# Performance work log

Hardware: AMD Instinct MI355X
Metric: run time of the kernel (lower is better)

The kernel has to match this reference:

```python
import jax, jax.numpy as jnp
import numpy as np

N_NODES = 50000
N_EDGES = 800000
F_IN, HID, N_CLS = 128, 64, 40


def gcn_conv(x, edge_index, W, b):
    """PyG GCNConv: add self-loops, symmetric normalization, linear, aggregate, bias."""
    n = x.shape[0]
    loop = jnp.arange(n, dtype=edge_index.dtype)
    src = jnp.concatenate([edge_index[0], loop])  # [E+N]
    dst = jnp.concatenate([edge_index[1], loop])  # [E+N]
    deg = jax.ops.segment_sum(jnp.ones_like(dst, dtype=x.dtype), dst, num_segments=n)
    dinv = jnp.where(deg > 0, jax.lax.rsqrt(deg), 0.0)
    norm = dinv[src] * dinv[dst]                   # [E+N]
    h = x @ W                                      # [N, out]
    out = jax.ops.segment_sum(h[src] * norm[:, None], dst, num_segments=n)
    return out + b


def setup_inputs() -> dict:
    key = jax.random.key(0)
    k1, k2, k3, k4 = jax.random.split(key, 4)
    x = jax.random.normal(k1, (N_NODES, F_IN), dtype=jnp.float32)
    edge_index = jax.random.randint(k2, (2, N_EDGES), 0, N_NODES, dtype=jnp.int32)
    W1 = jax.random.normal(k3, (F_IN, HID), dtype=jnp.float32) / np.sqrt(F_IN)
    b1 = jnp.zeros((HID,), dtype=jnp.float32)
    W2 = jax.random.normal(k4, (HID, N_CLS), dtype=jnp.float32) / np.sqrt(HID)
    b2 = jnp.zeros((N_CLS,), dtype=jnp.float32)
    return {"x": x, "edge_index": edge_index, "W1": W1, "b1": b1, "W2": W2, "b2": b2}


def reference(x, edge_index, W1, b1, W2, b2):
    # layer 1: GCNConv -> ReLU -> Dropout(eval = identity)
    h = jax.nn.relu(gcn_conv(x, edge_index, W1, b1))
    # layer 2: GCNConv -> ReLU -> Dropout(eval = identity); return_logits=True
    h = jax.nn.relu(gcn_conv(h, edge_index, W2, b2))
    return h
```

## Files before the change

### kernel.cpp

```cpp
#include <hip/hip_runtime.h>
#include <hip/hip_bf16.h>
#include <hip/hip_fp16.h>


#define N_FEAT_IN 128
#define N_HID 64
#define N_CLS 40

__device__ __forceinline__ float4 h4_to_f4(uint2 u) {
    __half2 a = *(__half2*)&u.x;
    __half2 b = *(__half2*)&u.y;
    float2 fa = __half22float2(a);
    float2 fb = __half22float2(b);
    return make_float4(fa.x, fa.y, fb.x, fb.y);
}

__device__ __forceinline__ uint2 f4_to_h4(float4 v) {
    uint2 w;
    *(__half2*)&w.x = __floats2half2_rn(v.x, v.y);
    *(__half2*)&w.y = __floats2half2_rn(v.z, v.w);
    return w;
}

__global__ void k_zero(int* a, int n) {
    int i = blockIdx.x * blockDim.x + threadIdx.x;
    if (i < n) a[i] = 0;
}

__global__ void k_count(const int* __restrict__ ei, int* deg, int* __restrict__ rank,
                        int E) {
    int e = blockIdx.x * blockDim.x + threadIdx.x;
    if (e < E) rank[e] = atomicAdd(&deg[ei[E + e]], 1);
}

__global__ void k_scan1(const int* __restrict__ deg, float* __restrict__ dinv,
                        int* incl, int* blksum, int n) {
    __shared__ int s[256];
    int i = blockIdx.x * 256 + threadIdx.x;
    int v = (i < n) ? deg[i] : 0;
    if (i < n) dinv[i] = 1.0f / sqrtf((float)(v + 1));
    s[threadIdx.x] = v;
    __syncthreads();
    for (int off = 1; off < 256; off <<= 1) {
        int t = (threadIdx.x >= off) ? s[threadIdx.x - off] : 0;
        __syncthreads();
        s[threadIdx.x] += t;
        __syncthreads();
    }
    if (i < n) incl[i] = s[threadIdx.x];
    if (threadIdx.x == 255) blksum[blockIdx.x] = s[255];
}

__global__ void k_scanB(const int* __restrict__ blksum, const int* __restrict__ incl,
                        const int* __restrict__ deg, int* __restrict__ row_start,
                        int nb, int n) {
    __shared__ int s[256];
    int t = threadIdx.x;
    int v = (t < nb) ? blksum[t] : 0;
    s[t] = v;
    __syncthreads();
    for (int off = 1; off < 256; off <<= 1) {
        int u = (t >= off) ? s[t - off] : 0;
        __syncthreads();
        s[t] += u;
        __syncthreads();
    }
    int bid = blockIdx.x;
    int blkoff = (bid == 0) ? 0 : s[bid - 1];
    int i = bid * 256 + t;
    if (i < n) row_start[i] = incl[i] - deg[i] + blkoff;
    if (bid == 0 && t == 0) row_start[n] = s[nb - 1];
}

__global__ __launch_bounds__(256) void k_g1_scatter2(
    const float* __restrict__ x, const float* __restrict__ W,
    const float* __restrict__ dinv, __half* __restrict__ hs, int n, int gb,
    const int* __restrict__ ei, const int* __restrict__ rank,
    const int* __restrict__ row_start, int* __restrict__ csr_src, int E) {
    __shared__ float Wl[64 * 64];
    __shared__ float Xs[64 * 68];
    int t = threadIdx.x;
    if (blockIdx.x >= gb) {
        int e = (blockIdx.x - gb) * 256 + t;
        if (e < E) {
            int s = ei[e];
            int d = ei[E + e];
            csr_src[row_start[d] + rank[e]] = s;
        }
        return;
    }
    int node0 = blockIdx.x * 64;
    int tn = t & 15;
    int tc = t >> 4;
    float acc[4][4] = {};
    for (int p = 0; p < 2; ++p) {
#pragma unroll
        for (int i = 0; i < 4; ++i) {
            int r = (t >> 4) + 16 * i;
            int c4 = t & 15;
            *(float4*)&Wl[r * 64 + c4 * 4] =
                *(const float4*)&W[(p * 64 + r) * N_HID + c4 * 4];
            int gr = node0 + r;
            float4 v = (gr < n)
                ? *(const float4*)&x[(size_t)gr * N_FEAT_IN + p * 64 + c4 * 4]
                : make_float4(0.f, 0.f, 0.f, 0.f);
            *(float4*)&Xs[r * 68 + c4 * 4] = v;
        }
        __syncthreads();
        for (int k = 0; k < 64; k += 4) {
            float4 xa[4], wb[4];
#pragma unroll
            for (int i = 0; i < 4; ++i)
                xa[i] = *(float4*)&Xs[(tn + 16 * i) * 68 + k];
#pragma unroll
            for (int kk = 0; kk < 4; ++kk)
                wb[kk] = *(float4*)&Wl[(k + kk) * 64 + tc * 4];
#pragma unroll
            for (int kk = 0; kk < 4; ++kk)
#pragma unroll
                for (int i = 0; i < 4; ++i)
#pragma unroll
                    for (int j = 0; j < 4; ++j)
                        acc[i][j] += ((const float*)&xa[i])[kk] * ((const float*)&wb[kk])[j];
        }
        __syncthreads();
    }
#pragma unroll
    for (int i = 0; i < 4; ++i) {
        int gr = node0 + tn + 16 * i;
        if (gr < n) {
            float di = dinv[gr];
            float4 v = make_float4(acc[i][0] * di, acc[i][1] * di,
                                   acc[i][2] * di, acc[i][3] * di);
            *(uint2*)(hs + (size_t)gr * N_HID + tc * 4) = f4_to_h4(v);
        }
    }
}

template <bool L1>
__global__ __launch_bounds__(256) void k_aggrh(const int* __restrict__ row_start,
                                               const int* __restrict__ csr_src,
                                               const float* __restrict__ dinv,
                                               const __half* __restrict__ hs,
                                               const float* __restrict__ b,
                                               void* __restrict__ outp, int n) {
    __shared__ int Ss[4 * 64];
    int wv = threadIdx.x >> 6, lane = threadIdx.x & 63;
    int g = lane >> 4, l = lane & 15;
    int node = blockIdx.x * 4 + wv;
    if (node >= n) return;
    float4 acc = make_float4(0.f, 0.f, 0.f, 0.f);
    if (g == 0) {
        uint2 u = *(const uint2*)(hs + (size_t)node * N_HID + l * 4);
        acc = h4_to_f4(u);
    }
    int beg = row_start[node], end = row_start[node + 1];
    for (int j0 = beg; j0 < end; j0 += 64) {
        int j = j0 + lane;
        if (j < end) Ss[wv * 64 + lane] = csr_src[j];
        int cnt = min(64, end - j0);
        int t = 0;
        for (; t + 16 <= cnt; t += 16) {
            int s1 = Ss[wv * 64 + t + g];
            int s2 = Ss[wv * 64 + t + 4 + g];
            int s3 = Ss[wv * 64 + t + 8 + g];
            int s4 = Ss[wv * 64 + t + 12 + g];
            uint2 u1 = *(const uint2*)(hs + (size_t)s1 * N_HID + l * 4);
            uint2 u2 = *(const uint2*)(hs + (size_t)s2 * N_HID + l * 4);
            uint2 u3 = *(const uint2*)(hs + (size_t)s3 * N_HID + l * 4);
            uint2 u4 = *(const uint2*)(hs + (size_t)s4 * N_HID + l * 4);
            float4 v1 = h4_to_f4(u1), v2 = h4_to_f4(u2);
            float4 v3 = h4_to_f4(u3), v4 = h4_to_f4(u4);
            acc.x += (v1.x + v2.x) + (v3.x + v4.x);
            acc.y += (v1.y + v2.y) + (v3.y + v4.y);
            acc.z += (v1.z + v2.z) + (v3.z + v4.z);
            acc.w += (v1.w + v2.w) + (v3.w + v4.w);
        }
        if (t + 8 <= cnt) {
            int s1 = Ss[wv * 64 + t + g];
            int s2 = Ss[wv * 64 + t + 4 + g];
            uint2 u1 = *(const uint2*)(hs + (size_t)s1 * N_HID + l * 4);
            uint2 u2 = *(const uint2*)(hs + (size_t)s2 * N_HID + l * 4);
            float4 v1 = h4_to_f4(u1), v2 = h4_to_f4(u2);
            acc.x += v1.x + v2.x; acc.y += v1.y + v2.y;
            acc.z += v1.z + v2.z; acc.w += v1.w + v2.w;
            t += 8;
        }
        for (; t < cnt; t += 4) {
            int e = t + g;
            if (e < cnt) {
                int s = Ss[wv * 64 + e];
                uint2 u = *(const uint2*)(hs + (size_t)s * N_HID + l * 4);
                float4 v = h4_to_f4(u);
                acc.x += v.x; acc.y += v.y; acc.z += v.z; acc.w += v.w;
            }
        }
    }
    acc.x += __shfl_xor(acc.x, 16); acc.y += __shfl_xor(acc.y, 16);
    acc.z += __shfl_xor(acc.z, 16); acc.w += __shfl_xor(acc.w, 16);
    acc.x += __shfl_xor(acc.x, 32); acc.y += __shfl_xor(acc.y, 32);
    acc.z += __shfl_xor(acc.z, 32); acc.w += __shfl_xor(acc.w, 32);
    if (g == 0) {
        float di = dinv[node];
        if (L1) {
            float4 bv = *(const float4*)&b[l * 4];
            float4 o;
            o.x = fmaxf(di * acc.x + bv.x, 0.f) * di;
            o.y = fmaxf(di * acc.y + bv.y, 0.f) * di;
            o.z = fmaxf(di * acc.z + bv.z, 0.f) * di;
            o.w = fmaxf(di * acc.w + bv.w, 0.f) * di;
            *(uint2*)((__half*)outp + (size_t)node * N_HID + l * 4) = f4_to_h4(o);
        } else {
            float4 o = make_float4(di * acc.x, di * acc.y, di * acc.z, di * acc.w);
            *(float4*)((float*)outp + (size_t)node * N_HID + l * 4) = o;
        }
    }
}

__global__ __launch_bounds__(256, 2) void k_gemm2f(const float* __restrict__ g2,
                                                   const float* __restrict__ W,
                                                   const float* __restrict__ bias,
                                                   float* __restrict__ out, int n) {
    __shared__ float Wl[N_HID * N_CLS];
    __shared__ float Xs[64 * 68];
    int t = threadIdx.x;
    int node0 = blockIdx.x * 64;
    for (int i = t * 4; i < N_HID * N_CLS; i += 1024)
        *(float4*)&Wl[i] = *(const float4*)&W[i];
#pragma unroll
    for (int i = 0; i < 4; ++i) {
        int r = (t >> 4) + i * 16;
        int c4 = t & 15;
        int gr = node0 + r;
        float4 v = (gr < n) ? *(const float4*)&g2[(size_t)gr * N_HID + c4 * 4]
                            : make_float4(0.f, 0.f, 0.f, 0.f);
        *(float4*)&Xs[r * 68 + c4 * 4] = v;
    }
    __syncthreads();
    int tn = t & 15;
    int tc = t >> 4;
    if (tc < 10) {
        float acc[4][4] = {};
        for (int k = 0; k < N_HID; k += 4) {
            float4 xa[4], wb[4];
#pragma unroll
            for (int i = 0; i < 4; ++i)
                xa[i] = *(float4*)&Xs[(tn + 16 * i) * 68 + k];
#pragma unroll
            for (int kk = 0; kk < 4; ++kk)
                wb[kk] = *(float4*)&Wl[(k + kk) * N_CLS + tc * 4];
#pragma unroll
            for (int kk = 0; kk < 4; ++kk)
#pragma unroll
                for (int i = 0; i < 4; ++i)
#pragma unroll
                    for (int j = 0; j < 4; ++j)
                        acc[i][j] += ((const float*)&xa[i])[kk] * ((const float*)&wb[kk])[j];
        }
        float4 bv = *(const float4*)&bias[tc * 4];
#pragma unroll
        for (int i = 0; i < 4; ++i) {
            int gr = node0 + tn + 16 * i;
            if (gr < n) {
                float4 v = make_float4(fmaxf(acc[i][0] + bv.x, 0.f),
                                       fmaxf(acc[i][1] + bv.y, 0.f),
                                       fmaxf(acc[i][2] + bv.z, 0.f),
                                       fmaxf(acc[i][3] + bv.w, 0.f));
                *(float4*)&out[(size_t)gr * N_CLS + tc * 4] = v;
            }
        }
    }
}

extern "C" void kernel_launch(void* const* d_in, const int* in_sizes, int n_in,
                              void* d_out, int out_size, void* d_ws, size_t ws_size,
                              hipStream_t stream) {
    const float* x = (const float*)d_in[0];
    const int* ei = (const int*)d_in[1];
    const float* W1 = (const float*)d_in[2];
    const float* b1 = (const float*)d_in[3];
    const float* W2 = (const float*)d_in[4];
    const float* b2 = (const float*)d_in[5];
    float* out = (float*)d_out;

    int n = in_sizes[0] / N_FEAT_IN;
    int E = in_sizes[1] / 2;
    int nb = (n + 255) / 256;

    char* ws = (char*)d_ws;
    float*  dinv      = (float*) (ws + 0);
    int*    deg_i     = (int*)   (ws + 200704);
    int*    row_start = (int*)   (ws + 401408);
    int*    incl      = (int*)   (ws + 602112);
    int*    blksum    = (int*)   (ws + 802816);
    int*    rank      = (int*)   (ws + 804864);
    int*    csr_src   = (int*)   (ws + 4004864);
    __half* h1s       = (__half*)(ws + 7204864);
    __half* out1s     = (__half*)(ws + 13604864);
    float*  g2d       = (float*) (ws + 20004864);

    const int B = 256;
    int gb = (n + 63) / 64;
    int cb = (E + 255) / 256;

    k_zero<<<(n + B - 1) / B, B, 0, stream>>>(deg_i, n);
    k_count<<<cb, B, 0, stream>>>(ei, deg_i, rank, E);
    k_scan1<<<nb, 256, 0, stream>>>(deg_i, dinv, incl, blksum, n);
    k_scanB<<<nb, 256, 0, stream>>>(blksum, incl, deg_i, row_start, nb, n);

    k_g1_scatter2<<<gb + cb, 256, 0, stream>>>(x, W1, dinv, h1s, n, gb,
                                               ei, rank, row_start, csr_src, E);

    k_aggrh<true><<<(n + 3) / 4, 256, 0, stream>>>(row_start, csr_src, dinv,
                                                   h1s, b1, (void*)out1s, n);
    k_aggrh<false><<<(n + 3) / 4, 256, 0, stream>>>(row_start, csr_src, dinv,
                                                    out1s, nullptr, (void*)g2d, n);
    k_gemm2f<<<gb, 256, 0, stream>>>(g2d, W2, b2, out, n);
}
```

Baseline: 130.5 us.

## Aggregate with 16-byte half loads, two nodes per wave, fp16 layer-2 intermediate

The aggregation kernel now gives each node a 32-lane half-wave, with each lane loading 8 halfs (uint4) instead of 4, so a wave processes two nodes. This cuts lane waste on short adjacency lists and makes the gathered loads wider. The second aggregation now writes fp16 into the reused h1s buffer instead of fp32, which halves that write and the GEMM read, at some loss of precision. The zero-fill kernel is replaced by hipMemsetAsync.

```diff
diff --git a/kernel.cpp b/kernel.cpp
--- a/kernel.cpp
+++ b/kernel.cpp
@@ -7,12 +7,23 @@
 #define N_HID 64
 #define N_CLS 40
 
-__device__ __forceinline__ float4 h4_to_f4(uint2 u) {
-    __half2 a = *(__half2*)&u.x;
-    __half2 b = *(__half2*)&u.y;
-    float2 fa = __half22float2(a);
-    float2 fb = __half22float2(b);
-    return make_float4(fa.x, fa.y, fb.x, fb.y);
+__device__ __forceinline__ void h8_acc(uint4 u, float4& a0, float4& a1) {
+    __half2* h = (__half2*)&u;
+    float2 f0 = __half22float2(h[0]);
+    float2 f1 = __half22float2(h[1]);
+    float2 f2 = __half22float2(h[2]);
+    float2 f3 = __half22float2(h[3]);
+    a0.x += f0.x; a0.y += f0.y; a0.z += f1.x; a0.w += f1.y;
+    a1.x += f2.x; a1.y += f2.y; a1.z += f3.x; a1.w += f3.y;
+}
+
+__device__ __forceinline__ uint4 f8_to_h8(float4 a0, float4 a1) {
+    uint4 u;
+    ((__half2*)&u)[0] = __floats2half2_rn(a0.x, a0.y);
+    ((__half2*)&u)[1] = __floats2half2_rn(a0.z, a0.w);
+    ((__half2*)&u)[2] = __floats2half2_rn(a1.x, a1.y);
+    ((__half2*)&u)[3] = __floats2half2_rn(a1.z, a1.w);
+    return u;
 }
 
 __device__ __forceinline__ uint2 f4_to_h4(float4 v) {
@@ -20,11 +31,6 @@
     *(__half2*)&w.x = __floats2half2_rn(v.x, v.y);
     *(__half2*)&w.y = __floats2half2_rn(v.z, v.w);
     return w;
-}
-
-__global__ void k_zero(int* a, int n) {
-    int i = blockIdx.x * blockDim.x + threadIdx.x;
-    if (i < n) a[i] = 0;
 }
 
 __global__ void k_count(const int* __restrict__ ei, int* deg, int* __restrict__ rank,
@@ -143,81 +149,82 @@
                                                const float* __restrict__ dinv,
                                                const __half* __restrict__ hs,
                                                const float* __restrict__ b,
-                                               void* __restrict__ outp, int n) {
-    __shared__ int Ss[4 * 64];
+                                               __half* __restrict__ outp, int n) {
+    __shared__ int Ss[4][2][32];
     int wv = threadIdx.x >> 6, lane = threadIdx.x & 63;
-    int g = lane >> 4, l = lane & 15;
-    int node = blockIdx.x * 4 + wv;
-    if (node >= n) return;
-    float4 acc = make_float4(0.f, 0.f, 0.f, 0.f);
-    if (g == 0) {
-        uint2 u = *(const uint2*)(hs + (size_t)node * N_HID + l * 4);
-        acc = h4_to_f4(u);
-    }
-    int beg = row_start[node], end = row_start[node + 1];
-    for (int j0 = beg; j0 < end; j0 += 64) {
-        int j = j0 + lane;
-        if (j < end) Ss[wv * 64 + lane] = csr_src[j];
-        int cnt = min(64, end - j0);
+    int hf = lane >> 5;
+    int hl = lane & 31;
+    int g = hl >> 3;
+    int l8 = hl & 7;
+    int node = blockIdx.x * 8 + wv * 2 + hf;
+    bool active = node < n;
+    float4 a0 = make_float4(0.f, 0.f, 0.f, 0.f);
+    float4 a1 = make_float4(0.f, 0.f, 0.f, 0.f);
+    if (active && g == 0) {
+        uint4 u = *(const uint4*)(hs + (size_t)node * N_HID + l8 * 8);
+        h8_acc(u, a0, a1);
+    }
+    int beg = 0, end = 0;
+    if (active) { beg = row_start[node]; end = row_start[node + 1]; }
+    for (int j0 = beg; j0 < end; j0 += 32) {
+        int j = j0 + hl;
+        if (j < end) Ss[wv][hf][hl] = csr_src[j];
+        int cnt = min(32, end - j0);
         int t = 0;
         for (; t + 16 <= cnt; t += 16) {
-            int s1 = Ss[wv * 64 + t + g];
-            int s2 = Ss[wv * 64 + t + 4 + g];
-            int s3 = Ss[wv * 64 + t + 8 + g];
-            int s4 = Ss[wv * 64 + t + 12 + g];
-            uint2 u1 = *(const uint2*)(hs + (size_t)s1 * N_HID + l * 4);
-            uint2 u2 = *(const uint2*)(hs + (size_t)s2 * N_HID + l * 4);
-            uint2 u3 = *(const uint2*)(hs + (size_t)s3 * N_HID + l * 4);
-            uint2 u4 = *(const uint2*)(hs + (size_t)s4 * N_HID + l * 4);
-            float4 v1 = h4_to_f4(u1), v2 = h4_to_f4(u2);
-            float4 v3 = h4_to_f4(u3), v4 = h4_to_f4(u4);
-            acc.x += (v1.x + v2.x) + (v3.x + v4.x);
-            acc.y += (v1.y + v2.y) + (v3.y + v4.y);
-            acc.z += (v1.z + v2.z) + (v3.z + v4.z);
-            acc.w += (v1.w + v2.w) + (v3.w + v4.w);
-        }
-        if (t + 8 <= cnt) {
-            int s1 = Ss[wv * 64 + t + g];
-            int s2 = Ss[wv * 64 + t + 4 + g];
-            uint2 u1 = *(const uint2*)(hs + (size_t)s1 * N_HID + l * 4);
-            uint2 u2 = *(const uint2*)(hs + (size_t)s2 * N_HID + l * 4);
-            float4 v1 = h4_to_f4(u1), v2 = h4_to_f4(u2);
-            acc.x += v1.x + v2.x; acc.y += v1.y + v2.y;
-            acc.z += v1.z + v2.z; acc.w += v1.w + v2.w;
-            t += 8;
+            int s1 = Ss[wv][hf][t + g];
+            int s2 = Ss[wv][hf][t + 4 + g];
+            int s3 = Ss[wv][hf][t + 8 + g];
+            int s4 = Ss[wv][hf][t + 12 + g];
+            uint4 u1 = *(const uint4*)(hs + (size_t)s1 * N_HID + l8 * 8);
+            uint4 u2 = *(const uint4*)(hs + (size_t)s2 * N_HID + l8 * 8);
+            uint4 u3 = *(const uint4*)(hs + (size_t)s3 * N_HID + l8 * 8);
+            uint4 u4 = *(const uint4*)(hs + (size_t)s4 * N_HID + l8 * 8);
+            h8_acc(u1, a0, a1);
+            h8_acc(u2, a0, a1);
+            h8_acc(u3, a0, a1);
+            h8_acc(u4, a0, a1);
         }
         for (; t < cnt; t += 4) {
             int e = t + g;
             if (e < cnt) {
-                int s = Ss[wv * 64 + e];
-                uint2 u = *(const uint2*)(hs + (size_t)s * N_HID + l * 4);
-                float4 v = h4_to_f4(u);
-                acc.x += v.x; acc.y += v.y; acc.z += v.z; acc.w += v.w;
+                int s = Ss[wv][hf][e];
+                uint4 u = *(const uint4*)(hs + (size_t)s * N_HID + l8 * 8);
+                h8_acc(u, a0, a1);
             }
         }
     }
-    acc.x += __shfl_xor(acc.x, 16); acc.y += __shfl_xor(acc.y, 16);
-    acc.z += __shfl_xor(acc.z, 16); acc.w += __shfl_xor(acc.w, 16);
-    acc.x += __shfl_xor(acc.x, 32); acc.y += __shfl_xor(acc.y, 32);
-    acc.z += __shfl_xor(acc.z, 32); acc.w += __shfl_xor(acc.w, 32);
-    if (g == 0) {
+    a0.x += __shfl_xor(a0.x, 8);  a0.y += __shfl_xor(a0.y, 8);
+    a0.z += __shfl_xor(a0.z, 8);  a0.w += __shfl_xor(a0.w, 8);
+    a1.x += __shfl_xor(a1.x, 8);  a1.y += __shfl_xor(a1.y, 8);
+    a1.z += __shfl_xor(a1.z, 8);  a1.w += __shfl_xor(a1.w, 8);
+    a0.x += __shfl_xor(a0.x, 16); a0.y += __shfl_xor(a0.y, 16);
+    a0.z += __shfl_xor(a0.z, 16); a0.w += __shfl_xor(a0.w, 16);
+    a1.x += __shfl_xor(a1.x, 16); a1.y += __shfl_xor(a1.y, 16);
+    a1.z += __shfl_xor(a1.z, 16); a1.w += __shfl_xor(a1.w, 16);
+    if (active && g == 0) {
         float di = dinv[node];
+        float4 o0, o1;
         if (L1) {
-            float4 bv = *(const float4*)&b[l * 4];
-            float4 o;
-            o.x = fmaxf(di * acc.x + bv.x, 0.f) * di;
-            o.y = fmaxf(di * acc.y + bv.y, 0.f) * di;
-            o.z = fmaxf(di * acc.z + bv.z, 0.f) * di;
-            o.w = fmaxf(di * acc.w + bv.w, 0.f) * di;
-            *(uint2*)((__half*)outp + (size_t)node * N_HID + l * 4) = f4_to_h4(o);
+            float4 b0 = *(const float4*)&b[l8 * 8];
+            float4 b1 = *(const float4*)&b[l8 * 8 + 4];
+            o0.x = fmaxf(di * a0.x + b0.x, 0.f) * di;
+            o0.y = fmaxf(di * a0.y + b0.y, 0.f) * di;
+            o0.z = fmaxf(di * a0.z + b0.z, 0.f) * di;
+            o0.w = fmaxf(di * a0.w + b0.w, 0.f) * di;
+            o1.x = fmaxf(di * a1.x + b1.x, 0.f) * di;
+            o1.y = fmaxf(di * a1.y + b1.y, 0.f) * di;
+            o1.z = fmaxf(di * a1.z + b1.z, 0.f) * di;
+            o1.w = fmaxf(di * a1.w + b1.w, 0.f) * di;
         } else {
-            float4 o = make_float4(di * acc.x, di * acc.y, di * acc.z, di * acc.w);
-            *(float4*)((float*)outp + (size_t)node * N_HID + l * 4) = o;
-        }
-    }
-}
-
-__global__ __launch_bounds__(256, 2) void k_gemm2f(const float* __restrict__ g2,
+            o0 = make_float4(di * a0.x, di * a0.y, di * a0.z, di * a0.w);
+            o1 = make_float4(di * a1.x, di * a1.y, di * a1.z, di * a1.w);
+        }
+        *(uint4*)(outp + (size_t)node * N_HID + l8 * 8) = f8_to_h8(o0, o1);
+    }
+}
+
+__global__ __launch_bounds__(256, 2) void k_gemm2f(const __half* __restrict__ g2,
                                                    const float* __restrict__ W,
                                                    const float* __restrict__ bias,
                                                    float* __restrict__ out, int n) {
@@ -228,13 +235,20 @@
     for (int i = t * 4; i < N_HID * N_CLS; i += 1024)
         *(float4*)&Wl[i] = *(const float4*)&W[i];
 #pragma unroll
-    for (int i = 0; i < 4; ++i) {
-        int r = (t >> 4) + i * 16;
-        int c4 = t & 15;
+    for (int q = 0; q < 2; ++q) {
+        int idx = q * 256 + t;
+        int r = idx >> 3, c8 = idx & 7;
         int gr = node0 + r;
-        float4 v = (gr < n) ? *(const float4*)&g2[(size_t)gr * N_HID + c4 * 4]
-                            : make_float4(0.f, 0.f, 0.f, 0.f);
-        *(float4*)&Xs[r * 68 + c4 * 4] = v;
+        uint4 u = make_uint4(0u, 0u, 0u, 0u);
+        if (gr < n) u = *(const uint4*)(g2 + (size_t)gr * N_HID + c8 * 8);
+        __half2* h = (__half2*)&u;
+        float2 f0 = __half22float2(h[0]);
+        float2 f1 = __half22float2(h[1]);
+        float2 f2 = __half22float2(h[2]);
+        float2 f3 = __half22float2(h[3]);
+        float* xp = &Xs[r * 68 + c8 * 8];
+        *(float4*)&xp[0] = make_float4(f0.x, f0.y, f1.x, f1.y);
+        *(float4*)&xp[4] = make_float4(f2.x, f2.y, f3.x, f3.y);
     }
     __syncthreads();
     int tn = t & 15;
@@ -297,13 +311,13 @@
     int*    csr_src   = (int*)   (ws + 4004864);
     __half* h1s       = (__half*)(ws + 7204864);
     __half* out1s     = (__half*)(ws + 13604864);
-    float*  g2d       = (float*) (ws + 20004864);
+    __half* g2h       = h1s;
 
     const int B = 256;
     int gb = (n + 63) / 64;
     int cb = (E + 255) / 256;
 
-    k_zero<<<(n + B - 1) / B, B, 0, stream>>>(deg_i, n);
+    hipMemsetAsync(deg_i, 0, (size_t)n * sizeof(int), stream);
     k_count<<<cb, B, 0, stream>>>(ei, deg_i, rank, E);
     k_scan1<<<nb, 256, 0, stream>>>(deg_i, dinv, incl, blksum, n);
     k_scanB<<<nb, 256, 0, stream>>>(blksum, incl, deg_i, row_start, nb, n);
@@ -311,9 +325,9 @@
     k_g1_scatter2<<<gb + cb, 256, 0, stream>>>(x, W1, dinv, h1s, n, gb,
                                                ei, rank, row_start, csr_src, E);
 
-    k_aggrh<true><<<(n + 3) / 4, 256, 0, stream>>>(row_start, csr_src, dinv,
-                                                   h1s, b1, (void*)out1s, n);
-    k_aggrh<false><<<(n + 3) / 4, 256, 0, stream>>>(row_start, csr_src, dinv,
-                                                    out1s, nullptr, (void*)g2d, n);
-    k_gemm2f<<<gb, 256, 0, stream>>>(g2d, W2, b2, out, n);
-}
+    k_aggrh<true><<<(n + 7) / 8, 256, 0, stream>>>(row_start, csr_src, dinv,
+                                                   h1s, b1, out1s, n);
+    k_aggrh<false><<<(n + 7) / 8, 256, 0, stream>>>(row_start, csr_src, dinv,
+                                                    out1s, nullptr, g2h, n);
+    k_gemm2f<<<gb, 256, 0, stream>>>(g2h, W2, b2, out, n);
+}
```

Measured after the change: 120.9 us. 1.08x faster.
